# Performance work log

Hardware: AMD Instinct MI355X
Metric: run time of the kernel (lower is better)

## Reference

```python
import math
import jax, jax.numpy as jnp
import numpy as np

CAPACITY_FACTOR = 1.25
MIN_CAPACITY = 4


def setup_inputs() -> dict:
    key = jax.random.key(0)
    k1, k2 = jax.random.split(key)
    inputs = jax.random.normal(k1, (8192, 64), dtype=jnp.float32)
    # replaces the module's internal Uniform(0,1).rsample for determinism
    rand = jax.random.uniform(k2, (8192, 64), dtype=jnp.float32)
    return {"inputs": inputs, "rand": rand}


def reference(inputs, rand):
    s, e = inputs.shape
    capacity = max(math.ceil(CAPACITY_FACTOR * s / e), MIN_CAPACITY)

    probs = jax.nn.softmax(inputs, axis=1)                      # [s, e]
    expert_idx = jnp.argmax(inputs, axis=1)                     # [s] (noisy_func is None)
    expert_mask = jax.nn.one_hot(expert_idx, e, dtype=inputs.dtype)  # [s, e]
    exp_counts = jnp.sum(expert_mask, axis=0).astype(jnp.int32)      # [e]

    # random tie-breaking capacity selection: top-`capacity` tokens per expert
    rand_mask = expert_mask * rand                              # [s, e]
    _, idx = jax.lax.top_k(rand_mask.T, capacity)               # idx: [e, c]
    keep = jnp.zeros((s, e), dtype=inputs.dtype).at[idx.T, jnp.arange(e)[None, :]].set(1.0)
    dispatch_mask = expert_mask * keep                          # [s, e]

    # position of each kept token within its expert's capacity slots
    loc = jnp.cumsum(dispatch_mask, axis=0) - 1.0               # [s, e]
    loc = jnp.sum(dispatch_mask * loc, axis=1).astype(jnp.int32)  # [s]
    loc_oh = jax.nn.one_hot(loc, capacity, dtype=inputs.dtype)  # [s, c]

    gated = probs * dispatch_mask                               # [s, e]
    combine_weights = gated[:, :, None] * loc_oh[:, None, :]    # [s, e, c]
    sec_mask = combine_weights.astype(bool)
    return combine_weights, sec_mask, exp_counts
```

## Files before the change

### kernel.cpp

```cpp
#include <hip/hip_runtime.h>

#define S 8192
#define E 64
#define CAP 160
static constexpr long long COMB = (long long)S * E * CAP;

__global__ __launch_bounds__(256) void router_kernel(
    const float* __restrict__ x, const float* __restrict__ rnd,
    int* __restrict__ eidx, float* __restrict__ prob, float* __restrict__ rv)
{
    const int token = blockIdx.x * 4 + (threadIdx.x >> 6);
    const int lane  = threadIdx.x & 63;

    const float v = x[token * E + lane];
    const float r = rnd[token * E + lane];

    float m = v; int ai = lane;
    #pragma unroll
    for (int off = 32; off; off >>= 1) {
        float m2 = __shfl_xor(m, off, 64);
        int   i2 = __shfl_xor(ai, off, 64);
        if (m2 > m || (m2 == m && i2 < ai)) { m = m2; ai = i2; }
    }

    float s = expf(v - m);
    #pragma unroll
    for (int off = 32; off; off >>= 1) s += __shfl_xor(s, off, 64);

    const float ra = __shfl(r, ai, 64);

    if (lane == 0) {
        eidx[token] = ai;
        prob[token] = 1.0f / s;
        rv[token]   = ra;
    }
}

__global__ __launch_bounds__(256) void dispatch_kernel(
    const int* __restrict__ eidx, const float* __restrict__ prob,
    const float* __restrict__ rv, float* __restrict__ out)
{
    const int e    = blockIdx.x;
    const int lane = threadIdx.x & 63;
    const int wave = threadIdx.x >> 6;

    __shared__ int s_count;
    __shared__ int s_run;
    __shared__ int wcnt[4];

    if (threadIdx.x == 0) { s_count = 0; s_run = 0; }
    __syncthreads();

    int local = 0;
    for (int t = threadIdx.x; t < S; t += 256) local += (eidx[t] == e);
    #pragma unroll
    for (int off = 32; off; off >>= 1) local += __shfl_xor(local, off, 64);
    if (lane == 0) atomicAdd(&s_count, local);
    __syncthreads();
    const int count = s_count;

    for (int base = 0; base < S; base += 256) {
        const int t = base + threadIdx.x;
        const bool match = (eidx[t] == e);
        bool kept = match;
        if (match && count > CAP) {
            int better = 0;
            const float rt = rv[t];
            for (int j = 0; j < S; ++j) {
                if (eidx[j] == e) {
                    const float rj = rv[j];
                    if (rj > rt || (rj == rt && j < t)) better++;
                }
            }
            kept = (better < CAP);
        }

        const unsigned long long bm = __ballot(kept);
        if (lane == 0) wcnt[wave] = __popcll(bm);
        __syncthreads();

        int loc = s_run + __popcll(bm & ((1ULL << lane) - 1ULL));
        for (int w = 0; w < wave; ++w) loc += wcnt[w];

        if (kept) {
            const long long p = ((long long)t * E + e) * CAP + loc;
            out[p]        = prob[t];
            out[COMB + p] = 1.0f;
        }
        __syncthreads();
        if (threadIdx.x == 0) s_run += wcnt[0] + wcnt[1] + wcnt[2] + wcnt[3];
        __syncthreads();
    }

    if (threadIdx.x == 0) out[2 * COMB + e] = (float)count;
}

extern "C" void kernel_launch(void* const* d_in, const int* in_sizes, int n_in,
                              void* d_out, int out_size, void* d_ws, size_t ws_size,
                              hipStream_t stream)
{
    const float* inputs = (const float*)d_in[0];
    const float* rnd    = (const float*)d_in[1];
    float* out = (float*)d_out;

    int*   eidx = (int*)d_ws;
    float* prob = (float*)((char*)d_ws + (size_t)S * sizeof(int));
    float* rv   = (float*)((char*)d_ws + (size_t)S * (sizeof(int) + sizeof(float)));

    hipMemsetAsync(d_out, 0, (size_t)out_size * sizeof(float), stream);

    router_kernel<<<S / 4, 256, 0, stream>>>(inputs, rnd, eidx, prob, rv);
    dispatch_kernel<<<E, 256, 0, stream>>>(eidx, prob, rv, out);
}
```

Before: 660.9 us.

## Replace memset plus sparse scatter with fused dense fill-scatter and parallel ranking

```diff
diff --git a/kernel.cpp b/kernel.cpp
--- a/kernel.cpp
+++ b/kernel.cpp
@@ -3,7 +3,11 @@
 #define S 8192
 #define E 64
 #define CAP 160
+#define ROW (E * CAP)
+#define NCHUNK (S / 256)
 static constexpr long long COMB = (long long)S * E * CAP;
+
+typedef float f32x4 __attribute__((ext_vector_type(4)));
 
 __global__ __launch_bounds__(256) void router_kernel(
     const float* __restrict__ x, const float* __restrict__ rnd,
@@ -36,63 +40,104 @@
     }
 }
 
-__global__ __launch_bounds__(256) void dispatch_kernel(
-    const int* __restrict__ eidx, const float* __restrict__ prob,
-    const float* __restrict__ rv, float* __restrict__ out)
+__global__ __launch_bounds__(256) void hist_kernel(
+    const int* __restrict__ eidx, int* __restrict__ chunk_hist)
 {
-    const int e    = blockIdx.x;
-    const int lane = threadIdx.x & 63;
-    const int wave = threadIdx.x >> 6;
+    __shared__ int h[E];
+    const int b = blockIdx.x;
+    if (threadIdx.x < E) h[threadIdx.x] = 0;
+    __syncthreads();
+    atomicAdd(&h[eidx[b * 256 + threadIdx.x]], 1);
+    __syncthreads();
+    if (threadIdx.x < E) chunk_hist[b * E + threadIdx.x] = h[threadIdx.x];
+}
 
-    __shared__ int s_count;
-    __shared__ int s_run;
-    __shared__ int wcnt[4];
+__global__ __launch_bounds__(256) void rank_kernel(
+    const int* __restrict__ eidx, const float* __restrict__ rv,
+    const int* __restrict__ chunk_hist,
+    int* __restrict__ ofs, int* __restrict__ counts_g)
+{
+    const int b   = blockIdx.x;
+    const int tid = threadIdx.x;
+    __shared__ int base[E];
+    __shared__ int tot[E];
+    __shared__ int le[256];
 
-    if (threadIdx.x == 0) { s_count = 0; s_run = 0; }
+    if (tid < E) {
+        int pre = 0, tt = 0;
+        for (int c = 0; c < NCHUNK; ++c) {
+            const int v = chunk_hist[c * E + tid];
+            if (c < b) pre += v;
+            tt += v;
+        }
+        base[tid] = pre; tot[tid] = tt;
+        if (b == 0) counts_g[tid] = tt;
+    }
+    const int t = b * 256 + tid;
+    const int e = eidx[t];
+    le[tid] = e;
     __syncthreads();
 
-    int local = 0;
-    for (int t = threadIdx.x; t < S; t += 256) local += (eidx[t] == e);
-    #pragma unroll
-    for (int off = 32; off; off >>= 1) local += __shfl_xor(local, off, 64);
-    if (lane == 0) atomicAdd(&s_count, local);
-    __syncthreads();
-    const int count = s_count;
+    int rank = 0;
+    for (int j = 0; j < tid; ++j) rank += (le[j] == e);
+    int loc = base[e] + rank;
 
-    for (int base = 0; base < S; base += 256) {
-        const int t = base + threadIdx.x;
-        const bool match = (eidx[t] == e);
-        bool kept = match;
-        if (match && count > CAP) {
-            int better = 0;
-            const float rt = rv[t];
-            for (int j = 0; j < S; ++j) {
+    bool kept = true;
+    if (tot[e] > CAP) {
+        const float rt = rv[t];
+        int better = 0;
+        for (int j = 0; j < S; ++j)
+            if (eidx[j] == e) {
+                const float rj = rv[j];
+                if (rj > rt || (rj == rt && j < t)) better++;
+            }
+        kept = (better < CAP);
+        if (kept) {
+            int l = 0;
+            for (int j = 0; j < t; ++j)
                 if (eidx[j] == e) {
                     const float rj = rv[j];
-                    if (rj > rt || (rj == rt && j < t)) better++;
+                    int bj = 0;
+                    for (int k = 0; k < S; ++k)
+                        if (eidx[k] == e) {
+                            const float rk = rv[k];
+                            if (rk > rj || (rk == rj && k < j)) bj++;
+                        }
+                    if (bj < CAP) l++;
                 }
-            }
-            kept = (better < CAP);
+            loc = l;
         }
+    }
+    ofs[t] = kept ? (e * CAP + loc) : -1;
+}
 
-        const unsigned long long bm = __ballot(kept);
-        if (lane == 0) wcnt[wave] = __popcll(bm);
-        __syncthreads();
+__global__ __launch_bounds__(256) void fill_scatter_kernel(
+    const int* __restrict__ ofs, const float* __restrict__ prob,
+    const int* __restrict__ counts, float* __restrict__ out)
+{
+    const int t   = blockIdx.x;
+    const int tid = threadIdx.x;
+    const int o   = ofs[t];
+    const float v = prob[t];
 
-        int loc = s_run + __popcll(bm & ((1ULL << lane) - 1ULL));
-        for (int w = 0; w < wave; ++w) loc += wcnt[w];
+    f32x4* __restrict__ dst0 = (f32x4*)(out + (size_t)t * ROW);
+    f32x4* __restrict__ dst1 = (f32x4*)(out + (size_t)COMB + (size_t)t * ROW);
 
-        if (kept) {
-            const long long p = ((long long)t * E + e) * CAP + loc;
-            out[p]        = prob[t];
-            out[COMB + p] = 1.0f;
-        }
-        __syncthreads();
-        if (threadIdx.x == 0) s_run += wcnt[0] + wcnt[1] + wcnt[2] + wcnt[3];
-        __syncthreads();
+    #pragma unroll
+    for (int k = 0; k < ROW / 4 / 256; ++k) {
+        const int c4  = k * 256 + tid;
+        const int col = c4 * 4;
+        f32x4 z0, z1;
+        z0.x = (o == col + 0) ? v : 0.0f;  z1.x = (o == col + 0) ? 1.0f : 0.0f;
+        z0.y = (o == col + 1) ? v : 0.0f;  z1.y = (o == col + 1) ? 1.0f : 0.0f;
+        z0.z = (o == col + 2) ? v : 0.0f;  z1.z = (o == col + 2) ? 1.0f : 0.0f;
+        z0.w = (o == col + 3) ? v : 0.0f;  z1.w = (o == col + 3) ? 1.0f : 0.0f;
+        __builtin_nontemporal_store(z0, &dst0[c4]);
+        __builtin_nontemporal_store(z1, &dst1[c4]);
     }
 
-    if (threadIdx.x == 0) out[2 * COMB + e] = (float)count;
+    if (t == 0 && tid < E)
+        out[2 * COMB + tid] = (float)counts[tid];
 }
 
 extern "C" void kernel_launch(void* const* d_in, const int* in_sizes, int n_in,
@@ -103,12 +148,16 @@
     const float* rnd    = (const float*)d_in[1];
     float* out = (float*)d_out;
 
-    int*   eidx = (int*)d_ws;
-    float* prob = (float*)((char*)d_ws + (size_t)S * sizeof(int));
-    float* rv   = (float*)((char*)d_ws + (size_t)S * (sizeof(int) + sizeof(float)));
-
-    hipMemsetAsync(d_out, 0, (size_t)out_size * sizeof(float), stream);
+    char* w = (char*)d_ws;
+    int*   eidx  = (int*)w;                          w += S * 4;
+    float* prob  = (float*)w;                        w += S * 4;
+    float* rv    = (float*)w;                        w += S * 4;
+    int*   ofs   = (int*)w;                          w += S * 4;
+    int*   chist = (int*)w;                          w += NCHUNK * E * 4;
+    int*   cnts  = (int*)w;
 
     router_kernel<<<S / 4, 256, 0, stream>>>(inputs, rnd, eidx, prob, rv);
-    dispatch_kernel<<<E, 256, 0, stream>>>(eidx, prob, rv, out);
+    hist_kernel<<<NCHUNK, 256, 0, stream>>>(eidx, chist);
+    rank_kernel<<<NCHUNK, 256, 0, stream>>>(eidx, rv, chist, ofs, cnts);
+    fill_scatter_kernel<<<S, 256, 0, stream>>>(ofs, prob, cnts, out);
 }
```

After: 660.8 us. Within noise of the previous version (-0.0%).
